# Performance work log

Hardware: AMD Instinct MI355X
Metric: run time of the kernel (lower is better)

Reference implementation:

```python
import jax, jax.numpy as jnp
import numpy as np

N_SRC = 100000
N_TGT = 100000
N_EDGES = 1600000
D = 128
HID = 128
OUT = 64
NUM_LAYERS = 2
P_DROP = 0.1
NEG_SLOPE = 0.01


def setup_inputs() -> dict:
    key = jax.random.key(0)
    ks = jax.random.split(key, 16)
    s = 1.0 / np.sqrt(D)
    inp = {
        "x_source": jax.random.normal(ks[0], (N_SRC, D), jnp.float32),
        "x_target": jax.random.normal(ks[1], (N_TGT, D), jnp.float32),
        "Wl_tgt": jax.random.normal(ks[2], (NUM_LAYERS, D, HID), jnp.float32) * s,
        "bl_tgt": jax.random.normal(ks[3], (NUM_LAYERS, HID), jnp.float32) * s,
        "Wr_tgt": jax.random.normal(ks[4], (NUM_LAYERS, D, HID), jnp.float32) * s,
        "Wl_src": jax.random.normal(ks[5], (NUM_LAYERS, D, HID), jnp.float32) * s,
        "bl_src": jax.random.normal(ks[6], (NUM_LAYERS, HID), jnp.float32) * s,
        "Wr_src": jax.random.normal(ks[7], (NUM_LAYERS, D, HID), jnp.float32) * s,
        "W_out": jax.random.normal(ks[8], (HID, OUT), jnp.float32) * (1.0 / np.sqrt(HID)),
        "b_out": jax.random.normal(ks[9], (OUT,), jnp.float32) * 0.01,
        "edge_src": jax.random.randint(ks[10], (N_EDGES,), 0, N_SRC, jnp.int32),
        "edge_dst": jax.random.randint(ks[11], (N_EDGES,), 0, N_TGT, jnp.int32),
        "rev_src": jax.random.randint(ks[12], (N_EDGES,), 0, N_TGT, jnp.int32),
        "rev_dst": jax.random.randint(ks[13], (N_EDGES,), 0, N_SRC, jnp.int32),
    }
    return inp


def _sage(x_src, x_dst, src_idx, dst_idx, n_dst, Wl, bl, Wr):
    # mean-aggregate neighbor messages per destination node (PyG SAGEConv default)
    msg = x_src[src_idx]  # [E, D] gather
    agg = jax.ops.segment_sum(msg, dst_idx, num_segments=n_dst)  # [n_dst, D]
    cnt = jax.ops.segment_sum(jnp.ones((src_idx.shape[0],), msg.dtype), dst_idx,
                              num_segments=n_dst)
    mean = agg / jnp.maximum(cnt, 1.0)[:, None]
    return mean @ Wl + bl + x_dst @ Wr


def _dropout(x, key):
    keep = jax.random.bernoulli(key, 1.0 - P_DROP, x.shape)
    return jnp.where(keep, x / (1.0 - P_DROP), jnp.zeros((), x.dtype))


def reference(x_source, x_target, Wl_tgt, bl_tgt, Wr_tgt, Wl_src, bl_src, Wr_src,
              W_out, b_out, edge_src, edge_dst, rev_src, rev_dst):
    dkey = jax.random.key(42)
    xs, xt = x_source, x_target
    for l in range(NUM_LAYERS):
        # ('source','edge','target'): target receives from source
        new_t = _sage(xs, xt, edge_src, edge_dst, N_TGT, Wl_tgt[l], bl_tgt[l], Wr_tgt[l])
        # ('target','rev_edge','source'): source receives from target
        new_s = _sage(xt, xs, rev_src, rev_dst, N_SRC, Wl_src[l], bl_src[l], Wr_src[l])
        new_t = jax.nn.leaky_relu(new_t, NEG_SLOPE)
        new_s = jax.nn.leaky_relu(new_s, NEG_SLOPE)
        new_t = _dropout(new_t, jax.random.fold_in(dkey, 2 * l))
        new_s = _dropout(new_s, jax.random.fold_in(dkey, 2 * l + 1))
        xs, xt = new_s, new_t
    return xs @ W_out + b_out
```

## Files before the change

### kernel.cpp

```cpp
#include <hip/hip_runtime.h>
#include <stdint.h>

#define NN 100000
#define NE 1600000
#define DD 128
#define XR 12500
#define PS 48

typedef unsigned short u16;
typedef short short8 __attribute__((ext_vector_type(8)));
typedef float floatx4 __attribute__((ext_vector_type(4)));
typedef int intx4 __attribute__((ext_vector_type(4)));

__device__ static inline u16 f2bf(float f){
  unsigned u = __float_as_uint(f);
  unsigned r = u + 0x7FFFu + ((u >> 16) & 1u);
  return (u16)(r >> 16);
}

__host__ __device__ static inline unsigned rotl32(unsigned x, int r){
  return (x << r) | (x >> (32 - r));
}

__host__ __device__ static inline void tf2x32(unsigned k0, unsigned k1,
                                              unsigned c0, unsigned c1,
                                              unsigned &o0, unsigned &o1)
{
  const unsigned ks2 = k0 ^ k1 ^ 0x1BD11BDAu;
  unsigned x0 = c0 + k0, x1 = c1 + k1;
#define TFR(r) { x0 += x1; x1 = rotl32(x1, (r)); x1 ^= x0; }
  TFR(13) TFR(15) TFR(26) TFR(6)   x0 += k1;  x1 += ks2 + 1u;
  TFR(17) TFR(29) TFR(16) TFR(24)  x0 += ks2; x1 += k0 + 2u;
  TFR(13) TFR(15) TFR(26) TFR(6)   x0 += k0;  x1 += k1 + 3u;
  TFR(17) TFR(29) TFR(16) TFR(24)  x0 += k1;  x1 += ks2 + 4u;
  TFR(13) TFR(15) TFR(26) TFR(6)   x0 += ks2; x1 += k0 + 5u;
#undef TFR
  o0 = x0; o1 = x1;
}

__device__ static inline float drop_scale(unsigned k0, unsigned k1, unsigned j)
{
  unsigned o0, o1;
  tf2x32(k0, k1, 0u, j, o0, o1);
  const unsigned bits = o0 ^ o1;
  const float u = __uint_as_float((bits >> 9) | 0x3F800000u) - 1.0f;
  return (u < 0.9f) ? (1.0f / 0.9f) : 0.0f;
}

__global__ __launch_bounds__(256) void k_fillp(const int* __restrict__ src,
                                               const int* __restrict__ dst,
                                               int* __restrict__ deg,
                                               int* __restrict__ csr){
  const int g = blockIdx.x & 7;
  const int j = blockIdx.x >> 3;
  const int NJ = gridDim.x >> 3;
  const int lo = g * XR, hi = lo + XR;
  for (int i = j * 256 + threadIdx.x; i < NE / 4; i += NJ * 256){
    intx4 d = __builtin_nontemporal_load((const intx4*)dst + i);
    intx4 s = __builtin_nontemporal_load((const intx4*)src + i);
    if (d.x >= lo && d.x < hi){ int p = atomicAdd(&deg[d.x], 1); if (p < PS) csr[d.x * PS + p] = s.x; }
    if (d.y >= lo && d.y < hi){ int p = atomicAdd(&deg[d.y], 1); if (p < PS) csr[d.y * PS + p] = s.y; }
    if (d.z >= lo && d.z < hi){ int p = atomicAdd(&deg[d.z], 1); if (p < PS) csr[d.z * PS + p] = s.z; }
    if (d.w >= lo && d.w < hi){ int p = atomicAdd(&deg[d.w], 1); if (p < PS) csr[d.w * PS + p] = s.w; }
  }
}

__global__ __launch_bounds__(256) void k_cvt(const float* __restrict__ in,
                                             u16* __restrict__ out, int n8){
  int i = blockIdx.x * 256 + threadIdx.x;
  if (i >= n8) return;
  floatx4 a = __builtin_nontemporal_load((const floatx4*)in + (size_t)i * 2);
  floatx4 b = __builtin_nontemporal_load((const floatx4*)in + (size_t)i * 2 + 1);
  u16 v[8] = { f2bf(a[0]), f2bf(a[1]), f2bf(a[2]), f2bf(a[3]),
               f2bf(b[0]), f2bf(b[1]), f2bf(b[2]), f2bf(b[3]) };
  *(uint4*)(out + (size_t)i * 8) = *(const uint4*)v;
}

__global__ __launch_bounds__(256) void k_prepW(const float* __restrict__ Wl,
                                               const float* __restrict__ Wr,
                                               u16* __restrict__ Wsw){
  int idx = blockIdx.x * 256 + threadIdx.x;
  int lane = idx & 63, tile = idx >> 6;
  int kt = tile >> 3, nt = tile & 7;
  int n = nt * 16 + (lane & 15);
  int kb = kt * 32 + (lane >> 4) * 8;
  u16 v[8];
  #pragma unroll
  for (int j = 0; j < 8; ++j){
    int k = kb + j;
    float w = (k < 128) ? Wl[(size_t)k * 128 + n] : Wr[(size_t)(k - 128) * 128 + n];
    v[j] = f2bf(w);
  }
  *(uint4*)(Wsw + (size_t)idx * 8) = *(const uint4*)v;
}

__global__ __launch_bounds__(256) void k_prepWo(const float* __restrict__ Wo,
                                                u16* __restrict__ Wsw){
  int idx = blockIdx.x * 256 + threadIdx.x;
  int lane = idx & 63, tile = idx >> 6;
  int kt = tile >> 2, nt = tile & 3;
  int n = nt * 16 + (lane & 15);
  int kb = kt * 32 + (lane >> 4) * 8;
  u16 v[8];
  #pragma unroll
  for (int j = 0; j < 8; ++j)
    v[j] = f2bf(Wo[(size_t)(kb + j) * 64 + n]);
  *(uint4*)(Wsw + (size_t)idx * 8) = *(const uint4*)v;
}

__global__ __launch_bounds__(256) void k_agg(const u16* __restrict__ x,
                                             const int* __restrict__ deg,
                                             const int* __restrict__ csr,
                                             u16* __restrict__ out){
  const int row  = blockIdx.x * 4 + (threadIdx.x >> 6);
  const int lane = threadIdx.x & 63;
  const int half = lane >> 5, l5 = lane & 31;
  int cnt = deg[row];
  if (cnt > PS) cnt = PS;
  const int beg = row * PS;
  float a0 = 0.f, a1 = 0.f, a2 = 0.f, a3 = 0.f;
  int e = 0;
  for (; e + 7 < cnt; e += 8){
    #pragma unroll
    for (int q = 0; q < 4; ++q){
      int s0 = csr[beg + e + 2 * q];
      int s1 = csr[beg + e + 2 * q + 1];
      int sm = half ? s1 : s0;
      uint2 v = *(const uint2*)(x + (size_t)sm * DD + l5 * 4);
      a0 += __uint_as_float(v.x << 16);
      a1 += __uint_as_float(v.x & 0xFFFF0000u);
      a2 += __uint_as_float(v.y << 16);
      a3 += __uint_as_float(v.y & 0xFFFF0000u);
    }
  }
  for (; e + 1 < cnt; e += 2){
    int s0 = csr[beg + e];
    int s1 = csr[beg + e + 1];
    int sm = half ? s1 : s0;
    uint2 v = *(const uint2*)(x + (size_t)sm * DD + l5 * 4);
    a0 += __uint_as_float(v.x << 16);
    a1 += __uint_as_float(v.x & 0xFFFF0000u);
    a2 += __uint_as_float(v.y << 16);
    a3 += __uint_as_float(v.y & 0xFFFF0000u);
  }
  if (e < cnt && half == 0){
    int sm = csr[beg + e];
    uint2 v = *(const uint2*)(x + (size_t)sm * DD + l5 * 4);
    a0 += __uint_as_float(v.x << 16);
    a1 += __uint_as_float(v.x & 0xFFFF0000u);
    a2 += __uint_as_float(v.y << 16);
    a3 += __uint_as_float(v.y & 0xFFFF0000u);
  }
  a0 += __shfl_xor(a0, 32);
  a1 += __shfl_xor(a1, 32);
  a2 += __shfl_xor(a2, 32);
  a3 += __shfl_xor(a3, 32);
  const float inv = (cnt > 0) ? (1.0f / (float)cnt) : 1.0f;
  if (half == 0){
    uint2 p;
    p.x = (unsigned)f2bf(a0 * inv) | ((unsigned)f2bf(a1 * inv) << 16);
    p.y = (unsigned)f2bf(a2 * inv) | ((unsigned)f2bf(a3 * inv) << 16);
    *(uint2*)(out + (size_t)row * DD + l5 * 4) = p;
  }
}

__global__ __launch_bounds__(256) void k_fused(const u16* __restrict__ Am,
    const u16* __restrict__ X, const u16* __restrict__ Wsw,
    const float* __restrict__ bias, u16* __restrict__ outH,
    unsigned key0, unsigned key1)
{
  const int wave = threadIdx.x >> 6, lane = threadIdx.x & 63;
  const int quad = lane >> 4, col0 = lane & 15;
  const int row0 = blockIdx.x * 64 + wave * 16;
  int m = row0 + col0;
  if (m >= NN) m = NN - 1;

  floatx4 acc[8];
  #pragma unroll
  for (int i = 0; i < 8; ++i) acc[i] = (floatx4)0.f;

  #pragma unroll
  for (int kt = 0; kt < 8; ++kt){
    const int k = kt * 32 + quad * 8;
    const u16* ap = (k < 128) ? (Am + (size_t)m * 128 + k)
                              : (X  + (size_t)m * 128 + (k - 128));
    short8 a = __builtin_nontemporal_load((const short8*)ap);
    #pragma unroll
    for (int nt = 0; nt < 8; ++nt){
      short8 b = *(const short8*)(Wsw + (size_t)(((kt * 8 + nt) * 64 + lane) * 8));
      acc[nt] = __builtin_amdgcn_mfma_f32_16x16x32_bf16(a, b, acc[nt], 0, 0, 0);
    }
  }

  #pragma unroll
  for (int nt = 0; nt < 8; ++nt){
    const int col = nt * 16 + col0;
    const float bj = bias[col];
    #pragma unroll
    for (int rg = 0; rg < 4; ++rg){
      const int r = row0 + quad * 4 + rg;
      if (r < NN){
        float h = acc[nt][rg] + bj;
        h = (h >= 0.f) ? h : 0.01f * h;
        unsigned j = (unsigned)r * 128u + (unsigned)col;
        h *= drop_scale(key0, key1, j);
        outH[(size_t)r * 128 + col] = f2bf(h);
      }
    }
  }
}

__global__ __launch_bounds__(256) void k_out(const u16* __restrict__ H,
    const u16* __restrict__ Wsw, const float* __restrict__ bias,
    float* __restrict__ out)
{
  const int wave = threadIdx.x >> 6, lane = threadIdx.x & 63;
  const int quad = lane >> 4, col0 = lane & 15;
  const int row0 = blockIdx.x * 64 + wave * 16;
  int m = row0 + col0;
  if (m >= NN) m = NN - 1;

  floatx4 acc[4];
  #pragma unroll
  for (int i = 0; i < 4; ++i) acc[i] = (floatx4)0.f;

  #pragma unroll
  for (int kt = 0; kt < 4; ++kt){
    short8 a = __builtin_nontemporal_load(
        (const short8*)(H + (size_t)m * 128 + kt * 32 + quad * 8));
    #pragma unroll
    for (int nt = 0; nt < 4; ++nt){
      short8 b = *(const short8*)(Wsw + (size_t)(((kt * 4 + nt) * 64 + lane) * 8));
      acc[nt] = __builtin_amdgcn_mfma_f32_16x16x32_bf16(a, b, acc[nt], 0, 0, 0);
    }
  }

  #pragma unroll
  for (int nt = 0; nt < 4; ++nt){
    const int col = nt * 16 + col0;
    const float bj = bias[col];
    #pragma unroll
    for (int rg = 0; rg < 4; ++rg){
      const int r = row0 + quad * 4 + rg;
      if (r < NN)
        out[(size_t)r * 64 + col] = acc[nt][rg] + bj;
    }
  }
}

extern "C" void kernel_launch(void* const* d_in, const int* in_sizes, int n_in,
                              void* d_out, int out_size, void* d_ws, size_t ws_size,
                              hipStream_t stream)
{
  const float* x_src  = (const float*)d_in[0];
  const float* x_tgt  = (const float*)d_in[1];
  const float* Wl_tgt = (const float*)d_in[2];
  const float* bl_tgt = (const float*)d_in[3];
  const float* Wr_tgt = (const float*)d_in[4];
  const float* Wl_src = (const float*)d_in[5];
  const float* bl_src = (const float*)d_in[6];
  const float* Wr_src = (const float*)d_in[7];
  const float* W_o    = (const float*)d_in[8];
  const float* b_o    = (const float*)d_in[9];
  const int*   e_src  = (const int*)d_in[10];
  const int*   e_dst  = (const int*)d_in[11];
  const int*   r_src  = (const int*)d_in[12];
  const int*   r_dst  = (const int*)d_in[13];
  float* out = (float*)d_out;
  (void)in_sizes; (void)n_in; (void)out_size; (void)ws_size;

  char* ws = (char*)d_ws;
  size_t off = 0;
  auto alloc = [&](size_t bytes) -> char* {
    char* p = ws + off; off += (bytes + 255) & ~(size_t)255; return p;
  };
  u16* Xs    = (u16*)alloc((size_t)NN * DD * 2);
  u16* Xt    = (u16*)alloc((size_t)NN * DD * 2);
  u16* A     = (u16*)alloc((size_t)NN * DD * 2);
  u16* B     = (u16*)alloc((size_t)NN * DD * 2);
  u16* C     = (u16*)alloc((size_t)NN * DD * 2);
  u16* Wsw0  = (u16*)alloc(256 * 128 * 2);
  u16* Wsw1  = (u16*)alloc(256 * 128 * 2);
  u16* Wsw2  = (u16*)alloc(256 * 128 * 2);
  u16* Wswo  = (u16*)alloc(128 * 64 * 2);
  int* deg_t = (int*)alloc((size_t)NN * 4);
  int* deg_s = (int*)alloc((size_t)NN * 4);
  int* csr_e = (int*)alloc((size_t)NN * PS * 4);
  int* csr_r = (int*)alloc((size_t)NN * PS * 4);

  unsigned kt0a, kt0b, ks0a, ks0b, ks1a, ks1b;
  tf2x32(0u, 42u, 0u, 0u, kt0a, kt0b);
  tf2x32(0u, 42u, 0u, 1u, ks0a, ks0b);
  tf2x32(0u, 42u, 0u, 3u, ks1a, ks1b);

  hipMemsetAsync(deg_t, 0, (size_t)NN * 4, stream);
  hipMemsetAsync(deg_s, 0, (size_t)NN * 4, stream);

  const int CB = (NN * DD / 8 + 255) / 256;
  const int PB = 8 * 256;

  k_cvt<<<CB, 256, 0, stream>>>(x_src, Xs, NN * DD / 8);
  k_cvt<<<CB, 256, 0, stream>>>(x_tgt, Xt, NN * DD / 8);
  k_prepW<<<16, 256, 0, stream>>>(Wl_tgt, Wr_tgt, Wsw0);
  k_prepW<<<16, 256, 0, stream>>>(Wl_src, Wr_src, Wsw1);
  k_prepW<<<16, 256, 0, stream>>>(Wl_src + 128 * 128, Wr_src + 128 * 128, Wsw2);
  k_prepWo<<<4, 256, 0, stream>>>(W_o, Wswo);

  k_fillp<<<PB, 256, 0, stream>>>(e_src, e_dst, deg_t, csr_e);
  k_fillp<<<PB, 256, 0, stream>>>(r_src, r_dst, deg_s, csr_r);

  const int GB = (NN + 63) / 64;
  const int AB = NN / 4;
  k_agg<<<AB, 256, 0, stream>>>(Xs, deg_t, csr_e, A);
  k_fused<<<GB, 256, 0, stream>>>(A, Xt, Wsw0, bl_tgt, B, kt0a, kt0b);
  k_agg<<<AB, 256, 0, stream>>>(Xt, deg_s, csr_r, A);
  k_fused<<<GB, 256, 0, stream>>>(A, Xs, Wsw1, bl_src, C, ks0a, ks0b);
  k_agg<<<AB, 256, 0, stream>>>(B, deg_s, csr_r, A);
  k_fused<<<GB, 256, 0, stream>>>(A, C, Wsw2, bl_src + 128, B, ks1a, ks1b);
  k_out<<<GB, 256, 0, stream>>>(B, Wswo, b_o, out);
}
```

Before: 676.8 us.

## Bucket edges by destination range before CSR fill; widen aggregation loads

The old per-range CSR fill made each of 8 block groups read the full edge list. It is replaced by a histogram, scan and scatter pass that bins packed edges into 8 destination-range buckets per direction, and a fill kernel that reads only its own bucket. The aggregation kernel now has each 16-lane group gather 16-byte rows, four edges in flight per wave, and reduces with two shuffles. Conversion and weight-prep launches are merged into fewer kernels. In exchange it adds extra kernels, a single-block scan and a staging buffer written and read once.

```diff
diff --git a/kernel.cpp b/kernel.cpp
--- a/kernel.cpp
+++ b/kernel.cpp
@@ -6,6 +6,7 @@
 #define DD 128
 #define XR 12500
 #define PS 48
+#define HB 1024
 
 typedef unsigned short u16;
 typedef short short8 __attribute__((ext_vector_type(8)));
@@ -47,28 +48,117 @@
   return (u < 0.9f) ? (1.0f / 0.9f) : 0.0f;
 }
 
-__global__ __launch_bounds__(256) void k_fillp(const int* __restrict__ src,
-                                               const int* __restrict__ dst,
+__global__ __launch_bounds__(256) void k_hist(const int* __restrict__ e_dst,
+                                              const int* __restrict__ r_dst,
+                                              int* __restrict__ hist){
+  __shared__ int h[16];
+  const int t = threadIdx.x;
+  if (t < 16) h[t] = 0;
+  __syncthreads();
+  const int QT = 2 * (NE / 4);
+  for (int i = blockIdx.x * 256 + t; i < QT; i += HB * 256){
+    int dir = (i >= NE / 4);
+    int qi = dir ? i - NE / 4 : i;
+    const int* dp = dir ? r_dst : e_dst;
+    intx4 d = __builtin_nontemporal_load((const intx4*)dp + qi);
+    int bb = dir << 3;
+    atomicAdd(&h[bb + d.x / XR], 1);
+    atomicAdd(&h[bb + d.y / XR], 1);
+    atomicAdd(&h[bb + d.z / XR], 1);
+    atomicAdd(&h[bb + d.w / XR], 1);
+  }
+  __syncthreads();
+  if (t < 16) hist[t * HB + blockIdx.x] = h[t];
+}
+
+__global__ __launch_bounds__(256) void k_scan(int* __restrict__ hist){
+  __shared__ int sh[16 * HB];
+  __shared__ int tot[256];
+  const int t = threadIdx.x;
+  const int N = 16 * HB;
+  for (int k = t; k < N; k += 256) sh[k] = hist[k];
+  __syncthreads();
+  int s = 0;
+  #pragma unroll 4
+  for (int k = 0; k < 64; ++k)
+    s += sh[(t >> 4) * HB + (t & 15) + (k << 4)];
+  tot[t] = s;
+  __syncthreads();
+  int v = s;
+  for (int off = 1; off < 256; off <<= 1){
+    int u = (t >= off) ? tot[t - off] : 0;
+    __syncthreads();
+    tot[t] += u;
+    __syncthreads();
+  }
+  int run = tot[t] - v;
+  for (int k = 0; k < 64; ++k){
+    int idx = (t >> 4) * HB + (t & 15) + (k << 4);
+    int xv = sh[idx];
+    sh[idx] = run;
+    run += xv;
+  }
+  __syncthreads();
+  for (int k = t; k < N; k += 256) hist[k] = sh[k];
+  if (t == 255) hist[N] = tot[255];
+}
+
+__global__ __launch_bounds__(256) void k_scatter(const int* __restrict__ e_src,
+                                                 const int* __restrict__ e_dst,
+                                                 const int* __restrict__ r_src,
+                                                 const int* __restrict__ r_dst,
+                                                 const int* __restrict__ base,
+                                                 unsigned* __restrict__ stage){
+  __shared__ int cur[16];
+  const int t = threadIdx.x;
+  if (t < 16) cur[t] = base[t * HB + blockIdx.x];
+  __syncthreads();
+  const int QT = 2 * (NE / 4);
+  for (int i = blockIdx.x * 256 + t; i < QT; i += HB * 256){
+    int dir = (i >= NE / 4);
+    int qi = dir ? i - NE / 4 : i;
+    const int* dp = dir ? r_dst : e_dst;
+    const int* sp = dir ? r_src : e_src;
+    intx4 d = __builtin_nontemporal_load((const intx4*)dp + qi);
+    intx4 sv = __builtin_nontemporal_load((const intx4*)sp + qi);
+    int bb = dir << 3;
+    int g, p;
+    g = d.x / XR; p = atomicAdd(&cur[bb + g], 1);
+    stage[p] = (unsigned)sv.x | ((unsigned)(d.x - g * XR) << 17);
+    g = d.y / XR; p = atomicAdd(&cur[bb + g], 1);
+    stage[p] = (unsigned)sv.y | ((unsigned)(d.y - g * XR) << 17);
+    g = d.z / XR; p = atomicAdd(&cur[bb + g], 1);
+    stage[p] = (unsigned)sv.z | ((unsigned)(d.z - g * XR) << 17);
+    g = d.w / XR; p = atomicAdd(&cur[bb + g], 1);
+    stage[p] = (unsigned)sv.w | ((unsigned)(d.w - g * XR) << 17);
+  }
+}
+
+__global__ __launch_bounds__(256) void k_fillb(const unsigned* __restrict__ stage,
+                                               const int* __restrict__ base,
                                                int* __restrict__ deg,
-                                               int* __restrict__ csr){
+                                               int* __restrict__ csr,
+                                               int dirbase){
   const int g = blockIdx.x & 7;
-  const int j = blockIdx.x >> 3;
-  const int NJ = gridDim.x >> 3;
-  const int lo = g * XR, hi = lo + XR;
-  for (int i = j * 256 + threadIdx.x; i < NE / 4; i += NJ * 256){
-    intx4 d = __builtin_nontemporal_load((const intx4*)dst + i);
-    intx4 s = __builtin_nontemporal_load((const intx4*)src + i);
-    if (d.x >= lo && d.x < hi){ int p = atomicAdd(&deg[d.x], 1); if (p < PS) csr[d.x * PS + p] = s.x; }
-    if (d.y >= lo && d.y < hi){ int p = atomicAdd(&deg[d.y], 1); if (p < PS) csr[d.y * PS + p] = s.y; }
-    if (d.z >= lo && d.z < hi){ int p = atomicAdd(&deg[d.z], 1); if (p < PS) csr[d.z * PS + p] = s.z; }
-    if (d.w >= lo && d.w < hi){ int p = atomicAdd(&deg[d.w], 1); if (p < PS) csr[d.w * PS + p] = s.w; }
-  }
-}
-
-__global__ __launch_bounds__(256) void k_cvt(const float* __restrict__ in,
-                                             u16* __restrict__ out, int n8){
+  const int j = blockIdx.x >> 3, NJ = gridDim.x >> 3;
+  const int bb = dirbase + g;
+  const int beg = base[bb * HB];
+  const int end = base[(bb + 1) * HB];
+  for (int i = beg + j * 256 + threadIdx.x; i < end; i += NJ * 256){
+    unsigned p = __builtin_nontemporal_load(stage + i);
+    int node = g * XR + (int)(p >> 17);
+    int pos = atomicAdd(&deg[node], 1);
+    if (pos < PS) csr[node * PS + pos] = (int)(p & 0x1FFFFu);
+  }
+}
+
+__global__ __launch_bounds__(256) void k_cvt2(const float* __restrict__ ina,
+                                              const float* __restrict__ inb,
+                                              u16* __restrict__ oa,
+                                              u16* __restrict__ ob, int n8){
   int i = blockIdx.x * 256 + threadIdx.x;
-  if (i >= n8) return;
+  const float* in = ina; u16* out = oa;
+  if (i >= n8){ i -= n8; in = inb; out = ob; }
   floatx4 a = __builtin_nontemporal_load((const floatx4*)in + (size_t)i * 2);
   floatx4 b = __builtin_nontemporal_load((const floatx4*)in + (size_t)i * 2 + 1);
   u16 v[8] = { f2bf(a[0]), f2bf(a[1]), f2bf(a[2]), f2bf(a[3]),
@@ -76,36 +166,42 @@
   *(uint4*)(out + (size_t)i * 8) = *(const uint4*)v;
 }
 
-__global__ __launch_bounds__(256) void k_prepW(const float* __restrict__ Wl,
-                                               const float* __restrict__ Wr,
-                                               u16* __restrict__ Wsw){
-  int idx = blockIdx.x * 256 + threadIdx.x;
-  int lane = idx & 63, tile = idx >> 6;
-  int kt = tile >> 3, nt = tile & 7;
-  int n = nt * 16 + (lane & 15);
-  int kb = kt * 32 + (lane >> 4) * 8;
-  u16 v[8];
-  #pragma unroll
-  for (int j = 0; j < 8; ++j){
-    int k = kb + j;
-    float w = (k < 128) ? Wl[(size_t)k * 128 + n] : Wr[(size_t)(k - 128) * 128 + n];
-    v[j] = f2bf(w);
-  }
-  *(uint4*)(Wsw + (size_t)idx * 8) = *(const uint4*)v;
-}
-
-__global__ __launch_bounds__(256) void k_prepWo(const float* __restrict__ Wo,
-                                                u16* __restrict__ Wsw){
-  int idx = blockIdx.x * 256 + threadIdx.x;
-  int lane = idx & 63, tile = idx >> 6;
-  int kt = tile >> 2, nt = tile & 3;
-  int n = nt * 16 + (lane & 15);
-  int kb = kt * 32 + (lane >> 4) * 8;
-  u16 v[8];
-  #pragma unroll
-  for (int j = 0; j < 8; ++j)
-    v[j] = f2bf(Wo[(size_t)(kb + j) * 64 + n]);
-  *(uint4*)(Wsw + (size_t)idx * 8) = *(const uint4*)v;
+__global__ __launch_bounds__(256) void k_prep(const float* __restrict__ Wl_tgt,
+    const float* __restrict__ Wr_tgt, const float* __restrict__ Wl_src,
+    const float* __restrict__ Wr_src, const float* __restrict__ Wo,
+    u16* __restrict__ Wsw0, u16* __restrict__ Wsw1, u16* __restrict__ Wsw2,
+    u16* __restrict__ Wswo){
+  int b = blockIdx.x;
+  if (b < 48){
+    const float *Wl, *Wr; u16* dst;
+    if (b < 16){ Wl = Wl_tgt; Wr = Wr_tgt; dst = Wsw0; }
+    else if (b < 32){ Wl = Wl_src; Wr = Wr_src; dst = Wsw1; b -= 16; }
+    else { Wl = Wl_src + 16384; Wr = Wr_src + 16384; dst = Wsw2; b -= 32; }
+    int idx = b * 256 + threadIdx.x;
+    int lane = idx & 63, tile = idx >> 6;
+    int kt = tile >> 3, nt = tile & 7;
+    int n = nt * 16 + (lane & 15);
+    int kb = kt * 32 + (lane >> 4) * 8;
+    u16 v[8];
+    #pragma unroll
+    for (int j = 0; j < 8; ++j){
+      int k = kb + j;
+      float w = (k < 128) ? Wl[(size_t)k * 128 + n] : Wr[(size_t)(k - 128) * 128 + n];
+      v[j] = f2bf(w);
+    }
+    *(uint4*)(dst + (size_t)idx * 8) = *(const uint4*)v;
+  } else {
+    int idx = (b - 48) * 256 + threadIdx.x;
+    int lane = idx & 63, tile = idx >> 6;
+    int kt = tile >> 2, nt = tile & 3;
+    int n = nt * 16 + (lane & 15);
+    int kb = kt * 32 + (lane >> 4) * 8;
+    u16 v[8];
+    #pragma unroll
+    for (int j = 0; j < 8; ++j)
+      v[j] = f2bf(Wo[(size_t)(kb + j) * 64 + n]);
+    *(uint4*)(Wswo + (size_t)idx * 8) = *(const uint4*)v;
+  }
 }
 
 __global__ __launch_bounds__(256) void k_agg(const u16* __restrict__ x,
@@ -114,53 +210,54 @@
                                              u16* __restrict__ out){
   const int row  = blockIdx.x * 4 + (threadIdx.x >> 6);
   const int lane = threadIdx.x & 63;
-  const int half = lane >> 5, l5 = lane & 31;
+  const int sub = lane >> 4, l4 = lane & 15;
   int cnt = deg[row];
   if (cnt > PS) cnt = PS;
   const int beg = row * PS;
-  float a0 = 0.f, a1 = 0.f, a2 = 0.f, a3 = 0.f;
+  float a[8] = {0.f,0.f,0.f,0.f,0.f,0.f,0.f,0.f};
   int e = 0;
   for (; e + 7 < cnt; e += 8){
-    #pragma unroll
-    for (int q = 0; q < 4; ++q){
-      int s0 = csr[beg + e + 2 * q];
-      int s1 = csr[beg + e + 2 * q + 1];
-      int sm = half ? s1 : s0;
-      uint2 v = *(const uint2*)(x + (size_t)sm * DD + l5 * 4);
-      a0 += __uint_as_float(v.x << 16);
-      a1 += __uint_as_float(v.x & 0xFFFF0000u);
-      a2 += __uint_as_float(v.y << 16);
-      a3 += __uint_as_float(v.y & 0xFFFF0000u);
-    }
-  }
-  for (; e + 1 < cnt; e += 2){
-    int s0 = csr[beg + e];
-    int s1 = csr[beg + e + 1];
-    int sm = half ? s1 : s0;
-    uint2 v = *(const uint2*)(x + (size_t)sm * DD + l5 * 4);
-    a0 += __uint_as_float(v.x << 16);
-    a1 += __uint_as_float(v.x & 0xFFFF0000u);
-    a2 += __uint_as_float(v.y << 16);
-    a3 += __uint_as_float(v.y & 0xFFFF0000u);
-  }
-  if (e < cnt && half == 0){
-    int sm = csr[beg + e];
-    uint2 v = *(const uint2*)(x + (size_t)sm * DD + l5 * 4);
-    a0 += __uint_as_float(v.x << 16);
-    a1 += __uint_as_float(v.x & 0xFFFF0000u);
-    a2 += __uint_as_float(v.y << 16);
-    a3 += __uint_as_float(v.y & 0xFFFF0000u);
-  }
-  a0 += __shfl_xor(a0, 32);
-  a1 += __shfl_xor(a1, 32);
-  a2 += __shfl_xor(a2, 32);
-  a3 += __shfl_xor(a3, 32);
+    int s0 = csr[beg + e + sub];
+    int s1 = csr[beg + e + 4 + sub];
+    uint4 v0 = *(const uint4*)(x + (size_t)s0 * DD + l4 * 8);
+    uint4 v1 = *(const uint4*)(x + (size_t)s1 * DD + l4 * 8);
+    a[0] += __uint_as_float(v0.x << 16); a[1] += __uint_as_float(v0.x & 0xFFFF0000u);
+    a[2] += __uint_as_float(v0.y << 16); a[3] += __uint_as_float(v0.y & 0xFFFF0000u);
+    a[4] += __uint_as_float(v0.z << 16); a[5] += __uint_as_float(v0.z & 0xFFFF0000u);
+    a[6] += __uint_as_float(v0.w << 16); a[7] += __uint_as_float(v0.w & 0xFFFF0000u);
+    a[0] += __uint_as_float(v1.x << 16); a[1] += __uint_as_float(v1.x & 0xFFFF0000u);
+    a[2] += __uint_as_float(v1.y << 16); a[3] += __uint_as_float(v1.y & 0xFFFF0000u);
+    a[4] += __uint_as_float(v1.z << 16); a[5] += __uint_as_float(v1.z & 0xFFFF0000u);
+    a[6] += __uint_as_float(v1.w << 16); a[7] += __uint_as_float(v1.w & 0xFFFF0000u);
+  }
+  for (; e + 3 < cnt; e += 4){
+    int s0 = csr[beg + e + sub];
+    uint4 v0 = *(const uint4*)(x + (size_t)s0 * DD + l4 * 8);
+    a[0] += __uint_as_float(v0.x << 16); a[1] += __uint_as_float(v0.x & 0xFFFF0000u);
+    a[2] += __uint_as_float(v0.y << 16); a[3] += __uint_as_float(v0.y & 0xFFFF0000u);
+    a[4] += __uint_as_float(v0.z << 16); a[5] += __uint_as_float(v0.z & 0xFFFF0000u);
+    a[6] += __uint_as_float(v0.w << 16); a[7] += __uint_as_float(v0.w & 0xFFFF0000u);
+  }
+  if (e + sub < cnt){
+    int s0 = csr[beg + e + sub];
+    uint4 v0 = *(const uint4*)(x + (size_t)s0 * DD + l4 * 8);
+    a[0] += __uint_as_float(v0.x << 16); a[1] += __uint_as_float(v0.x & 0xFFFF0000u);
+    a[2] += __uint_as_float(v0.y << 16); a[3] += __uint_as_float(v0.y & 0xFFFF0000u);
+    a[4] += __uint_as_float(v0.z << 16); a[5] += __uint_as_float(v0.z & 0xFFFF0000u);
+    a[6] += __uint_as_float(v0.w << 16); a[7] += __uint_as_float(v0.w & 0xFFFF0000u);
+  }
+  #pragma unroll
+  for (int i = 0; i < 8; ++i){
+    a[i] += __shfl_xor(a[i], 16);
+    a[i] += __shfl_xor(a[i], 32);
+  }
   const float inv = (cnt > 0) ? (1.0f / (float)cnt) : 1.0f;
-  if (half == 0){
-    uint2 p;
-    p.x = (unsigned)f2bf(a0 * inv) | ((unsigned)f2bf(a1 * inv) << 16);
-    p.y = (unsigned)f2bf(a2 * inv) | ((unsigned)f2bf(a3 * inv) << 16);
-    *(uint2*)(out + (size_t)row * DD + l5 * 4) = p;
+  if (sub == 0){
+    unsigned pk[4];
+    #pragma unroll
+    for (int i = 0; i < 4; ++i)
+      pk[i] = (unsigned)f2bf(a[2*i] * inv) | ((unsigned)f2bf(a[2*i+1] * inv) << 16);
+    *(uint4*)(out + (size_t)row * DD + l4 * 8) = make_uint4(pk[0], pk[1], pk[2], pk[3]);
   }
 }
 
@@ -283,31 +380,32 @@
   u16* Wsw1  = (u16*)alloc(256 * 128 * 2);
   u16* Wsw2  = (u16*)alloc(256 * 128 * 2);
   u16* Wswo  = (u16*)alloc(128 * 64 * 2);
-  int* deg_t = (int*)alloc((size_t)NN * 4);
-  int* deg_s = (int*)alloc((size_t)NN * 4);
+  int* deg   = (int*)alloc((size_t)2 * NN * 4);
+  int* deg_t = deg;
+  int* deg_s = deg + NN;
   int* csr_e = (int*)alloc((size_t)NN * PS * 4);
   int* csr_r = (int*)alloc((size_t)NN * PS * 4);
+  int* hist  = (int*)alloc((size_t)(16 * HB + 1) * 4);
+  unsigned* stage = (unsigned*)alloc((size_t)2 * NE * 4);
 
   unsigned kt0a, kt0b, ks0a, ks0b, ks1a, ks1b;
   tf2x32(0u, 42u, 0u, 0u, kt0a, kt0b);
   tf2x32(0u, 42u, 0u, 1u, ks0a, ks0b);
   tf2x32(0u, 42u, 0u, 3u, ks1a, ks1b);
 
-  hipMemsetAsync(deg_t, 0, (size_t)NN * 4, stream);
-  hipMemsetAsync(deg_s, 0, (size_t)NN * 4, stream);
-
-  const int CB = (NN * DD / 8 + 255) / 256;
-  const int PB = 8 * 256;
-
-  k_cvt<<<CB, 256, 0, stream>>>(x_src, Xs, NN * DD / 8);
-  k_cvt<<<CB, 256, 0, stream>>>(x_tgt, Xt, NN * DD / 8);
-  k_prepW<<<16, 256, 0, stream>>>(Wl_tgt, Wr_tgt, Wsw0);
-  k_prepW<<<16, 256, 0, stream>>>(Wl_src, Wr_src, Wsw1);
-  k_prepW<<<16, 256, 0, stream>>>(Wl_src + 128 * 128, Wr_src + 128 * 128, Wsw2);
-  k_prepWo<<<4, 256, 0, stream>>>(W_o, Wswo);
-
-  k_fillp<<<PB, 256, 0, stream>>>(e_src, e_dst, deg_t, csr_e);
-  k_fillp<<<PB, 256, 0, stream>>>(r_src, r_dst, deg_s, csr_r);
+  hipMemsetAsync(deg, 0, (size_t)2 * NN * 4, stream);
+
+  const int CB = NN * DD / 8 / 256;
+
+  k_cvt2<<<2 * CB, 256, 0, stream>>>(x_src, x_tgt, Xs, Xt, NN * DD / 8);
+  k_prep<<<52, 256, 0, stream>>>(Wl_tgt, Wr_tgt, Wl_src, Wr_src, W_o,
+                                 Wsw0, Wsw1, Wsw2, Wswo);
+
+  k_hist<<<HB, 256, 0, stream>>>(e_dst, r_dst, hist);
+  k_scan<<<1, 256, 0, stream>>>(hist);
+  k_scatter<<<HB, 256, 0, stream>>>(e_src, e_dst, r_src, r_dst, hist, stage);
+  k_fillb<<<8 * 32, 256, 0, stream>>>(stage, hist, deg_t, csr_e, 0);
+  k_fillb<<<8 * 32, 256, 0, stream>>>(stage, hist, deg_s, csr_r, 8);
 
   const int GB = (NN + 63) / 64;
   const int AB = NN / 4;
```

Result: faster. 657.1 us (-2.9%).
